# Performance work log

Hardware: AMD Instinct MI355X
Metric: run time of the kernel (lower is better)

Reference implementation:

```python
import jax, jax.numpy as jnp
import numpy as np

B, S, H, A, E, ED, RH = 16, 2048, 1024, 32, 8, 256, 128  # batch, seq, hidden, act_dim, num_experts, expert_dim, router/aux hidden

def _mk(key, shape, scale=0.02):
    return (jax.random.normal(key, shape, dtype=jnp.float32) * scale)

def setup_inputs() -> dict:
    key = jax.random.key(0)
    ks = jax.random.split(key, 20)
    inp = {
        "state_rep": jax.random.normal(ks[0], (B, S, H), dtype=jnp.float32),
        "base_action": jax.random.normal(ks[1], (B, S, A), dtype=jnp.float32),
        "attention_mask": jnp.ones((B, S), dtype=jnp.float32),
        # shared expert
        "sw1": _mk(ks[2], (H, ED)), "sb1": jnp.zeros((ED,), jnp.float32),
        "sw2": _mk(ks[3], (ED, A)), "sb2": jnp.zeros((A,), jnp.float32),
        # stacked specialized experts
        "ew1": _mk(ks[4], (E, H, ED)), "eb1": jnp.zeros((E, ED), jnp.float32),
        "ew2": _mk(ks[5], (E, ED, A)), "eb2": jnp.zeros((E, A), jnp.float32),
        # router
        "rw1": _mk(ks[6], (H, RH)), "rb1": jnp.zeros((RH,), jnp.float32),
        "rw2": _mk(ks[7], (RH, E)), "rb2": jnp.zeros((E,), jnp.float32),
        # residual mlp
        "mw1": _mk(ks[8], (A, RH)), "mb1": jnp.zeros((RH,), jnp.float32),
        "mw2": _mk(ks[9], (RH, A)), "mb2": jnp.zeros((A,), jnp.float32),
        # value estimator
        "vw1": _mk(ks[10], (H, RH)), "vb1": jnp.zeros((RH,), jnp.float32),
        "vw2": _mk(ks[11], (RH, 1)), "vb2": jnp.zeros((1,), jnp.float32),
    }
    return inp

def reference(state_rep, base_action, attention_mask,
              sw1, sb1, sw2, sb2, ew1, eb1, ew2, eb2,
              rw1, rb1, rw2, rb2, mw1, mb1, mw2, mb2,
              vw1, vb1, vw2, vb2):
    gelu = lambda x: jax.nn.gelu(x, approximate=False)  # torch nn.GELU default (erf)
    # value estimator -> sigmoid RTG  [B,S,1]
    return_rtg = jax.nn.sigmoid(jax.nn.relu(state_rep @ vw1 + vb1) @ vw2 + vb2)
    # shared expert [B,S,A]
    shared_output = gelu(state_rep @ sw1 + sb1) @ sw2 + sb2
    # candidate actions [B,S,E,A]
    scaling = jnp.linspace(0.8, 1.2, E, dtype=jnp.float32).reshape(1, 1, E, 1)
    candidate_actions = base_action[:, :, None, :] * scaling
    # router softmax [B,S,E]
    router_logits = gelu(state_rep @ rw1 + rb1) @ rw2 + rb2
    selection_probs = jax.nn.softmax(router_logits, axis=-1)
    # all experts on all tokens (matches the training-mode torch loop)
    h1 = gelu(jnp.einsum('bsh,ehd->bsed', state_rep, ew1) + eb1[None, None, :, :])
    expert_outputs = jnp.einsum('bsed,eda->bsea', h1, ew2) + eb2[None, None, :, :]
    # training branch: soft combine
    weighted_expert = jnp.sum(selection_probs[..., None] * expert_outputs, axis=2)
    moe_output = shared_output + weighted_expert
    residual = gelu(moe_output @ mw1 + mb1) @ mw2 + mb2
    final_action = weighted_expert + residual
    final_action = final_action * attention_mask[..., None]
    return (final_action, candidate_actions, selection_probs, return_rtg)
```

## Files before the change

kernel.cpp:

```cpp
#include <hip/hip_runtime.h>
#include <stdint.h>

#define T_TOT 32768
#define H_DIM 1024
#define A_DIM 32
#define E_NUM 8
#define ED_DIM 256
#define RH_DIM 128
#define NBIG 2560
#define K2 2304

typedef float f32x4 __attribute__((ext_vector_type(4)));
typedef short bf16x8 __attribute__((ext_vector_type(8)));
typedef unsigned short u16;
typedef u16 u16x8 __attribute__((ext_vector_type(8)));

typedef uint32_t __attribute__((address_space(1))) as1_u32;
typedef uint32_t __attribute__((address_space(3))) as3_u32;

__device__ __forceinline__ u16 f2bf(float f) {
    union { float f; uint32_t u; } v; v.f = f;
    return (u16)((v.u + 0x7FFFu + ((v.u >> 16) & 1u)) >> 16);
}
__device__ __forceinline__ float bf2f(u16 h) {
    union { uint32_t u; float f; } v; v.u = ((uint32_t)h) << 16;
    return v.f;
}
__device__ __forceinline__ float gelu_fast(float x) {
    const float x2 = x * x;
    const float s = x * fmaf(0.07135481627f, x2, 1.5957691216f);
    const float e = __expf(-s);
    return x * __builtin_amdgcn_rcpf(1.0f + e);
}
__device__ __forceinline__ void gload_lds16(const void* g, void* lds) {
    __builtin_amdgcn_global_load_lds((const as1_u32*)(uintptr_t)g,
                                     (as3_u32*)(uintptr_t)lds, 16, 0, 0);
}


__global__ void k_packwt(const float* __restrict__ ew1, const float* __restrict__ sw1,
                         const float* __restrict__ rw1, const float* __restrict__ vw1,
                         u16* __restrict__ wbf) {
    __shared__ float t[64][65];
    const int nt = blockIdx.x >> 4, kt = blockIdx.x & 15;
    const int n0 = nt * 64, k0 = kt * 64;
    const int tx = threadIdx.x & 63, ty = threadIdx.x >> 6;
#pragma unroll 4
    for (int it = 0; it < 16; ++it) {
        const int k = k0 + ty + it * 4;
        const int n = n0 + tx;
        float v;
        if (n0 < 2048)      v = ew1[(size_t)((n0 >> 8) * H_DIM + k) * ED_DIM + (n & 255)];
        else if (n0 < 2304) v = sw1[(size_t)k * ED_DIM + (n - 2048)];
        else if (n0 < 2432) v = rw1[(size_t)k * RH_DIM + (n - 2304)];
        else                v = vw1[(size_t)k * RH_DIM + (n - 2432)];
        t[ty + it * 4][tx] = v;
    }
    __syncthreads();
#pragma unroll 4
    for (int it = 0; it < 16; ++it) {
        const int nl = ty + it * 4;
        wbf[(size_t)(n0 + nl) * H_DIM + k0 + tx] = f2bf(t[tx][nl]);
    }
}


#define SB_W2T (A_DIM * K2)
#define SB_W1B (SB_W2T + 4096)
#define SB_W2B (SB_W1B + 4352)
#define SB_BIA (SB_W2B + NBIG)
#define SB_CND (SB_BIA + T_TOT * E_NUM * A_DIM)

__global__ void k_setup(const float* __restrict__ eb1, const float* __restrict__ sb1,
                        const float* __restrict__ rb1, const float* __restrict__ vb1,
                        const float* __restrict__ ew2, const float* __restrict__ sw2,
                        const float* __restrict__ mw1, const float* __restrict__ mw2,
                        const float* __restrict__ base, const float* __restrict__ state,
                        float* __restrict__ biascat,
                        u16* __restrict__ w2t, u16* __restrict__ w1b, u16* __restrict__ w2b,
                        float* __restrict__ cand_out, u16* __restrict__ xb, int nconv4) {
    int i = blockIdx.x * blockDim.x + threadIdx.x;
    if (i < SB_W2T) {
        int a = i / K2, d = i - a * K2;
        float v = (d < 2048) ? ew2[(size_t)d * A_DIM + a] : sw2[(size_t)(d - 2048) * A_DIM + a];
        w2t[i] = f2bf(v);
    } else if (i < SB_W1B) {
        int t = i - SB_W2T;
        w1b[t] = f2bf(mw1[t]);
    } else if (i < SB_W2B) {
        int t = i - SB_W1B;
        int c = t / 136, j = t - c * 136;
        w2b[t] = (j < RH_DIM) ? f2bf(mw2[(size_t)j * A_DIM + c]) : (u16)0;
    } else if (i < SB_BIA) {
        int n = i - SB_W2B;
        float b;
        if (n < 2048)      b = eb1[(n >> 8) * ED_DIM + (n & 255)];
        else if (n < 2304) b = sb1[n - 2048];
        else if (n < 2432) b = rb1[n - 2304];
        else               b = vb1[n - 2432];
        biascat[n] = b;
    } else if (i < SB_CND) {
        int t = i - SB_BIA;
        int a = t & 31, e = (t >> 5) & 7, tt = t >> 8;
        cand_out[t] = base[(size_t)tt * A_DIM + a] * (0.8f + 0.4f * (float)e / 7.0f);
    } else if (i < SB_CND + nconv4) {
        int t = i - SB_CND;
        float4 v = ((const float4*)state)[t];
        ushort4 o;
        o.x = f2bf(v.x); o.y = f2bf(v.y); o.z = f2bf(v.z); o.w = f2bf(v.w);
        ((ushort4*)xb)[t] = o;
    }
}

__global__ void k_convert_x(const float* __restrict__ x, u16* __restrict__ xb, int n4) {
    int i = blockIdx.x * blockDim.x + threadIdx.x;
    if (i >= n4) return;
    float4 v = ((const float4*)x)[i];
    ushort4 o;
    o.x = f2bf(v.x); o.y = f2bf(v.y); o.z = f2bf(v.z); o.w = f2bf(v.w);
    ((ushort4*)xb)[i] = o;
}


#define SLOT 8192

__launch_bounds__(512, 2)
__global__ void k_gemm1(const u16* __restrict__ xb, const u16* __restrict__ wbf,
                        const float* __restrict__ biascat, const u16* __restrict__ w2t,
                        float* __restrict__ Pb,
                        const float* __restrict__ rw2, const float* __restrict__ rb2,
                        const float* __restrict__ vw2, const float* __restrict__ vb2,
                        float* __restrict__ probs_out, float* __restrict__ rtg_out) {
    __shared__ u16 smem[8 * SLOT];
    __shared__ float rw2s[RH_DIM * E_NUM];
    __shared__ float vws[RH_DIM];
    __shared__ float rb2s[E_NUM];
    const int tid = threadIdx.x;
    const int wid = tid >> 6;
    const int lane = tid & 63;
    const int lin = blockIdx.x;
    const int swz = (lin & 7) * ((int)gridDim.x >> 3) + (lin >> 3);
    const int bx = swz % 10;
    const int by = swz / 10;
    const int m0 = by * 256, n0 = bx * 256;
    const int wr = wid >> 2;
    const int wc = wid & 3;
    const int srow = tid >> 3;
    const int cs = 8 * ((tid & 7) ^ (srow & 7));
    const int l15 = lane & 15;
    const int rsw = (lane & 7) * 8;
    const int lh8 = (lane >> 4) * 8;
    const int c0 = lh8 ^ rsw;
    const int c1 = (32 + lh8) ^ rsw;
    const int aRd = (wr * 16 + l15) * 64;
    const int bRd = ((wc & 1) * 64 + l15) * 64;
    const int bSlotHi = wc >> 1;

    f32x4 acc[8][4];
#pragma unroll
    for (int j = 0; j < 8; ++j)
#pragma unroll
        for (int n = 0; n < 4; ++n) acc[j][n] = (f32x4){0.f, 0.f, 0.f, 0.f};

    auto stageA = [&](int h, int kt, int s) {
        const u16* src = xb + (size_t)(m0 + h * 128 + srow) * H_DIM + kt * 64 + cs;
        u16* dst = smem + s * SLOT + wid * 512;
        gload_lds16(src, dst);
        gload_lds16(src + (size_t)64 * H_DIM, dst + 4096);
    };
    auto stageB = [&](int h, int kt, int s) {
        const u16* src = wbf + (size_t)(n0 + h * 128 + srow) * H_DIM + kt * 64 + cs;
        u16* dst = smem + s * SLOT + wid * 512;
        gload_lds16(src, dst);
        gload_lds16(src + (size_t)64 * H_DIM, dst + 4096);
    };

    bf16x8 bfr[4][2];

#define G1_READA(q, P, A0, A1)                                                    \
    {                                                                             \
        const u16* ab0 = smem + ((P) * 4 + ((q) >> 1)) * SLOT + aRd + (((2*(q)) & 3) * 2048);     \
        const u16* ab1 = smem + ((P) * 4 + ((q) >> 1)) * SLOT + aRd + (((2*(q)+1) & 3) * 2048);   \
        A0[0] = *(const bf16x8*)&ab0[c0]; A0[1] = *(const bf16x8*)&ab0[c1];       \
        A1[0] = *(const bf16x8*)&ab1[c0]; A1[1] = *(const bf16x8*)&ab1[c1];       \
    }

#define G1_MFMA(q, A0, A1)                                                        \
    _Pragma("unroll")                                                             \
    for (int ni = 0; ni < 4; ++ni) {                                              \
        acc[2*(q)][ni]   = __builtin_amdgcn_mfma_f32_16x16x32_bf16(A0[0], bfr[ni][0], acc[2*(q)][ni], 0, 0, 0);   \
        acc[2*(q)][ni]   = __builtin_amdgcn_mfma_f32_16x16x32_bf16(A0[1], bfr[ni][1], acc[2*(q)][ni], 0, 0, 0);   \
        acc[2*(q)+1][ni] = __builtin_amdgcn_mfma_f32_16x16x32_bf16(A1[0], bfr[ni][0], acc[2*(q)+1][ni], 0, 0, 0); \
        acc[2*(q)+1][ni] = __builtin_amdgcn_mfma_f32_16x16x32_bf16(A1[1], bfr[ni][1], acc[2*(q)+1][ni], 0, 0, 0); \
    }

    stageB(0, 0, 2); stageB(1, 0, 3);
    stageA(0, 0, 0); stageA(1, 0, 1);
    stageB(0, 1, 6); stageB(1, 1, 7);
    asm volatile("s_waitcnt vmcnt(6)" ::: "memory");
    __builtin_amdgcn_s_barrier();

#pragma unroll 2
    for (int kt = 0; kt < 16; ++kt) {
        const int p = kt & 1;
        const int ktA = (kt + 1) & 15;
        const int ktB = (kt + 2) & 15;
        const int pA = ktA & 1;
        bf16x8 a0[2], a1[2];
        G1_READA(0, p, a0, a1)
#pragma unroll
        for (int ni = 0; ni < 4; ++ni) {
            const u16* bb = smem + (p * 4 + 2 + bSlotHi) * SLOT + bRd + ni * 1024;
            bfr[ni][0] = *(const bf16x8*)&bb[c0];
            bfr[ni][1] = *(const bf16x8*)&bb[c1];
        }
        stageA(0, ktA, pA * 4);
        __builtin_amdgcn_s_barrier();
        asm volatile("s_waitcnt lgkmcnt(0)" ::: "memory");
        __builtin_amdgcn_sched_barrier(0);
        __builtin_amdgcn_s_setprio(1);
        G1_MFMA(0, a0, a1)
        __builtin_amdgcn_s_setprio(0);
        G1_READA(1, p, a0, a1)
        stageA(1, ktA, pA * 4 + 1);
        asm volatile("s_waitcnt vmcnt(8)" ::: "memory");
        __builtin_amdgcn_s_barrier();
        asm volatile("s_waitcnt lgkmcnt(0)" ::: "memory");
        __builtin_amdgcn_sched_barrier(0);
        __builtin_amdgcn_s_setprio(1);
        G1_MFMA(1, a0, a1)
        __builtin_amdgcn_s_setprio(0);
        G1_READA(2, p, a0, a1)
        stageB(0, ktB, p * 4 + 2);
        __builtin_amdgcn_s_barrier();
        asm volatile("s_waitcnt lgkmcnt(0)" ::: "memory");
        __builtin_amdgcn_sched_barrier(0);
        __builtin_amdgcn_s_setprio(1);
        G1_MFMA(2, a0, a1)
        __builtin_amdgcn_s_setprio(0);
        G1_READA(3, p, a0, a1)
        stageB(1, ktB, p * 4 + 3);
        asm volatile("s_waitcnt vmcnt(6)" ::: "memory");
        __builtin_amdgcn_s_barrier();
        asm volatile("s_waitcnt lgkmcnt(0)" ::: "memory");
        __builtin_amdgcn_sched_barrier(0);
        __builtin_amdgcn_s_setprio(1);
        G1_MFMA(3, a0, a1)
        __builtin_amdgcn_s_setprio(0);
    }
#undef G1_READA
#undef G1_MFMA

    const int crow = (lane >> 4) * 4;
    __syncthreads();
    if (bx != 9) {
#pragma unroll
        for (int j = 0; j < 8; ++j) {
#pragma unroll
            for (int ni = 0; ni < 4; ++ni) {
                const int col = wc * 64 + ni * 16 + l15;
                const float bias = biascat[n0 + col];
#pragma unroll
                for (int r = 0; r < 4; ++r) {
                    const int row = wr * 16 + j * 32 + crow + r;
                    const float v = gelu_fast(acc[j][ni][r] + bias);
                    smem[row * 256 + ((((col >> 3) ^ (row & 15)) << 3) | (col & 7))] = f2bf(v);
                }
            }
        }
        __syncthreads();
        f32x4 accP[2][2];
#pragma unroll
        for (int m = 0; m < 2; ++m)
#pragma unroll
            for (int n = 0; n < 2; ++n) accP[m][n] = (f32x4){0.f, 0.f, 0.f, 0.f};
        const int lh16 = lane >> 4;
#pragma unroll
        for (int g = 0; g < 8; ++g) {
            bf16x8 bv[2], av[2];
#pragma unroll
            for (int ni = 0; ni < 2; ++ni)
                bv[ni] = *(const bf16x8*)(w2t + (size_t)(ni * 16 + l15) * K2 + n0 + g * 32 + lh16 * 8);
#pragma unroll
            for (int m = 0; m < 2; ++m) {
                const int row = wid * 32 + m * 16 + l15;
                av[m] = *(const bf16x8*)&smem[row * 256 + (((g * 4 + lh16) ^ l15) << 3)];
            }
#pragma unroll
            for (int m = 0; m < 2; ++m)
#pragma unroll
                for (int ni = 0; ni < 2; ++ni)
                    accP[m][ni] = __builtin_amdgcn_mfma_f32_16x16x32_bf16(av[m], bv[ni], accP[m][ni], 0, 0, 0);
        }
#pragma unroll
        for (int m = 0; m < 2; ++m)
#pragma unroll
            for (int ni = 0; ni < 2; ++ni)
#pragma unroll
                for (int r = 0; r < 4; ++r) {
                    const int row = m0 + wid * 32 + m * 16 + crow + r;
                    Pb[((size_t)row * 9 + bx) * 32 + ni * 16 + l15] = accP[m][ni][r];
                }
    } else {
        for (int i = tid; i < RH_DIM * E_NUM; i += 512) rw2s[i] = rw2[i];
        if (tid < RH_DIM) vws[tid] = vw2[tid];
        if (tid < E_NUM) rb2s[tid] = rb2[tid];
        char* sb = (char*)smem;
#pragma unroll
        for (int j = 0; j < 8; ++j) {
#pragma unroll
            for (int ni = 0; ni < 4; ++ni) {
                const int col = wc * 64 + ni * 16 + l15;
                const float bias = biascat[2304 + col];
#pragma unroll
                for (int r = 0; r < 4; ++r) {
                    const int row = wr * 16 + j * 32 + crow + r;
                    float v = acc[j][ni][r] + bias;
                    v = (col < 128) ? gelu_fast(v) : fmaxf(v, 0.f);
                    *(u16*)(sb + row * 512 + ((col * 2) ^ ((row & 31) << 4))) = f2bf(v);
                }
            }
        }
        __syncthreads();
        if (tid < 256) {
            const int row = tid;
            float lg[E_NUM];
#pragma unroll
            for (int e = 0; e < E_NUM; ++e) lg[e] = rb2s[e];
            const int rx = (row & 31) << 4;
#pragma unroll 4
            for (int s = 0; s < 16; ++s) {
                u16x8 v8 = *(const u16x8*)(sb + row * 512 + ((s << 4) ^ rx));
#pragma unroll
                for (int q = 0; q < 8; ++q) {
                    const float xv = bf2f(v8[q]);
                    const float* wr8 = &rw2s[(s * 8 + q) * E_NUM];
#pragma unroll
                    for (int e = 0; e < E_NUM; ++e) lg[e] = fmaf(xv, wr8[e], lg[e]);
                }
            }
            float mx = lg[0];
#pragma unroll
            for (int e = 1; e < E_NUM; ++e) mx = fmaxf(mx, lg[e]);
            float sm = 0.f;
            float ex[E_NUM];
#pragma unroll
            for (int e = 0; e < E_NUM; ++e) { ex[e] = __expf(lg[e] - mx); sm += ex[e]; }
            const float rs = 1.0f / sm;
#pragma unroll
            for (int e = 0; e < E_NUM; ++e) probs_out[(size_t)(m0 + row) * E_NUM + e] = ex[e] * rs;
        } else {
            const int row = tid - 256;
            const int rx = (row & 31) << 4;
            float pv = 0.f;
#pragma unroll 4
            for (int s = 16; s < 32; ++s) {
                u16x8 v8 = *(const u16x8*)(sb + row * 512 + ((s << 4) ^ rx));
#pragma unroll
                for (int q = 0; q < 8; ++q) pv = fmaf(bf2f(v8[q]), vws[(s - 16) * 8 + q], pv);
            }
            rtg_out[m0 + row] = 1.f / (1.f + __expf(-(pv + vb2[0])));
        }
    }
}


__launch_bounds__(256, 3)
__global__ void k_combine(const float* __restrict__ Pb, const float* __restrict__ probs,
                          const float* __restrict__ eb2, const float* __restrict__ sb2,
                          const u16* __restrict__ w1b, const u16* __restrict__ w2b,
                          const float* __restrict__ mb1, const float* __restrict__ mb2,
                          const float* __restrict__ mask, float* __restrict__ out_final) {
    __shared__ float plds[64 * E_NUM];
    __shared__ u16 Am[64 * 40];
    __shared__ u16 rhm[64 * 136];
    __shared__ u16 w1s[32 * 128];
    __shared__ u16 w2s[32 * 136];
    const int tid = threadIdx.x;
    const int wid = tid >> 6;
    const int lane = tid & 63;
    const int m0 = blockIdx.x * 64;
    const int crow = (lane >> 4) * 4;
    const int ccol = lane & 15;

    for (int i = tid; i < 64 * E_NUM; i += 256) plds[i] = probs[(size_t)m0 * E_NUM + i];
    for (int i = tid; i < 4096; i += 256) w1s[i] = w1b[i];
    for (int i = tid; i < 544; i += 256) *(u16x8*)&w2s[i * 8] = *(const u16x8*)&w2b[i * 8];
    __syncthreads();

    float wgt[2][4];
#pragma unroll
    for (int n = 0; n < 2; ++n) {
        const int aIdx = n * 16 + ccol;
#pragma unroll
        for (int r = 0; r < 4; ++r) {
            const int row = wid * 16 + crow + r;
            const float* pt = Pb + (size_t)(m0 + row) * 288;
            float w = 0.f;
#pragma unroll
            for (int e = 0; e < E_NUM; ++e)
                w = fmaf(plds[row * E_NUM + e], pt[e * 32 + aIdx] + eb2[e * A_DIM + aIdx], w);
            wgt[n][r] = w;
            Am[row * 40 + aIdx] = f2bf(w + pt[256 + aIdx] + sb2[aIdx]);
        }
    }
    __syncthreads();
    {
        const int row = tid >> 2, seg = tid & 3;
        float mrow[32];
#pragma unroll
        for (int a = 0; a < 32; ++a) mrow[a] = bf2f(Am[row * 40 + a]);
#pragma unroll 4
        for (int jj = 0; jj < 32; ++jj) {
            const int j = seg * 32 + jj;
            float s = mb1[j];
#pragma unroll
            for (int a = 0; a < 32; ++a) s = fmaf(mrow[a], bf2f(w1s[a * 128 + j]), s);
            rhm[row * 136 + j] = f2bf(gelu_fast(s));
        }
    }
    __syncthreads();
#pragma unroll
    for (int n = 0; n < 2; ++n) {
        const int aIdx = n * 16 + ccol;
        const float b2 = mb2[aIdx];
#pragma unroll
        for (int r = 0; r < 4; ++r) {
            const int row = wid * 16 + crow + r;
            float s = b2;
#pragma unroll
            for (int jc = 0; jc < 16; ++jc) {
                u16x8 rv = *(const u16x8*)&rhm[row * 136 + jc * 8];
                u16x8 wv = *(const u16x8*)&w2s[aIdx * 136 + jc * 8];
#pragma unroll
                for (int q = 0; q < 8; ++q) s = fmaf(bf2f(rv[q]), bf2f(wv[q]), s);
            }
            const int t = m0 + row;
            out_final[(size_t)t * A_DIM + aIdx] = (wgt[n][r] + s) * mask[t];
        }
    }
}


extern "C" void kernel_launch(void* const* d_in, const int* in_sizes, int n_in,
                              void* d_out, int out_size, void* d_ws, size_t ws_size,
                              hipStream_t stream) {
    const float* state = (const float*)d_in[0];
    const float* base  = (const float*)d_in[1];
    const float* mask  = (const float*)d_in[2];
    const float* sw1 = (const float*)d_in[3];
    const float* sb1 = (const float*)d_in[4];
    const float* sw2 = (const float*)d_in[5];
    const float* sb2 = (const float*)d_in[6];
    const float* ew1 = (const float*)d_in[7];
    const float* eb1 = (const float*)d_in[8];
    const float* ew2 = (const float*)d_in[9];
    const float* eb2 = (const float*)d_in[10];
    const float* rw1 = (const float*)d_in[11];
    const float* rb1 = (const float*)d_in[12];
    const float* rw2 = (const float*)d_in[13];
    const float* rb2 = (const float*)d_in[14];
    const float* mw1 = (const float*)d_in[15];
    const float* mb1 = (const float*)d_in[16];
    const float* mw2 = (const float*)d_in[17];
    const float* mb2 = (const float*)d_in[18];
    const float* vw1 = (const float*)d_in[19];
    const float* vb1 = (const float*)d_in[20];
    const float* vw2 = (const float*)d_in[21];
    const float* vb2 = (const float*)d_in[22];

    float* out_final = (float*)d_out;
    float* out_cand  = out_final + 1048576;
    float* out_probs = out_final + 9437184;
    float* out_rtg   = out_final + 9699328;

    auto al = [](size_t b) { return (b + 255) & ~(size_t)255; };
    auto need = [&](size_t T) {
        return al((size_t)NBIG * H_DIM * 2) + al((size_t)A_DIM * K2 * 2) + al((size_t)NBIG * 4)
             + al((size_t)4096 * 2) + al((size_t)4352 * 2)
             + al(T * H_DIM * 2) + al(T * 9 * A_DIM * 4);
    };
    size_t Tc = 8192;
    if (need(32768) <= ws_size)      Tc = 32768;
    else if (need(16384) <= ws_size) Tc = 16384;
    const int nchunk = (int)(T_TOT / Tc);

    char* ws = (char*)d_ws;
    size_t off = 0;
    auto take = [&](size_t b) { char* p = ws + off; off += (b + 255) & ~(size_t)255; return p; };
    u16*   wbf   = (u16*)take((size_t)NBIG * H_DIM * 2);
    u16*   w2t   = (u16*)take((size_t)A_DIM * K2 * 2);
    float* bias  = (float*)take((size_t)NBIG * 4);
    u16*   w1b   = (u16*)take((size_t)4096 * 2);
    u16*   w2b   = (u16*)take((size_t)4352 * 2);
    u16*   xb    = (u16*)take(Tc * H_DIM * 2);
    float* Pb    = (float*)take(Tc * 9 * A_DIM * 4);
    (void)in_sizes; (void)n_in; (void)out_size;

    const int nconv4 = (Tc == 32768) ? (T_TOT * H_DIM / 4) : 0;
    const int ntot = SB_CND + nconv4;
    k_packwt<<<640, 256, 0, stream>>>(ew1, sw1, rw1, vw1, wbf);
    k_setup<<<(ntot + 255) / 256, 256, 0, stream>>>(
        eb1, sb1, rb1, vb1, ew2, sw2, mw1, mw2,
        base, state, bias, w2t, w1b, w2b, out_cand, xb, nconv4);

    for (int c = 0; c < nchunk; ++c) {
        const size_t tb = (size_t)c * Tc;
        if (nconv4 == 0)
            k_convert_x<<<(int)(Tc * H_DIM / 4 / 256), 256, 0, stream>>>(state + tb * H_DIM, xb, (int)(Tc * H_DIM / 4));
        k_gemm1<<<10 * (int)(Tc / 256), 512, 0, stream>>>(xb, wbf, bias, w2t, Pb,
                                                          rw2, rb2, vw2, vb2,
                                                          out_probs + tb * E_NUM, out_rtg + tb);
        k_combine<<<(int)(Tc / 64), 256, 0, stream>>>(Pb, out_probs + tb * E_NUM, eb2, sb2,
                                                      w1b, w2b, mb1, mb2, mask + tb, out_final + tb * A_DIM);
    }
}
```

Measured before the change: 274.8 us.

## Merge weight packing into setup, vectorize conversions, store expert partials as bf16

Folds the weight transpose/pack kernel into the setup kernel as extra blocks, which removes one launch and lets both run concurrently. The candidate-action and state-to-bf16 conversion loops now handle 4 and 8 elements per thread. The intermediate per-expert partial outputs buffer is stored as bf16 instead of fp32, halving its write and read traffic between the GEMM and combine kernels. The trade-off is extra rounding on the expert outputs before the weighted combine.

After: 251.3 us. 8.6% less time.

```diff
diff --git a/kernel.cpp b/kernel.cpp
--- a/kernel.cpp
+++ b/kernel.cpp
@@ -38,77 +38,84 @@
 }
 
 
-__global__ void k_packwt(const float* __restrict__ ew1, const float* __restrict__ sw1,
-                         const float* __restrict__ rw1, const float* __restrict__ vw1,
-                         u16* __restrict__ wbf) {
-    __shared__ float t[64][65];
-    const int nt = blockIdx.x >> 4, kt = blockIdx.x & 15;
-    const int n0 = nt * 64, k0 = kt * 64;
-    const int tx = threadIdx.x & 63, ty = threadIdx.x >> 6;
-#pragma unroll 4
-    for (int it = 0; it < 16; ++it) {
-        const int k = k0 + ty + it * 4;
-        const int n = n0 + tx;
-        float v;
-        if (n0 < 2048)      v = ew1[(size_t)((n0 >> 8) * H_DIM + k) * ED_DIM + (n & 255)];
-        else if (n0 < 2304) v = sw1[(size_t)k * ED_DIM + (n - 2048)];
-        else if (n0 < 2432) v = rw1[(size_t)k * RH_DIM + (n - 2304)];
-        else                v = vw1[(size_t)k * RH_DIM + (n - 2432)];
-        t[ty + it * 4][tx] = v;
-    }
-    __syncthreads();
-#pragma unroll 4
-    for (int it = 0; it < 16; ++it) {
-        const int nl = ty + it * 4;
-        wbf[(size_t)(n0 + nl) * H_DIM + k0 + tx] = f2bf(t[tx][nl]);
-    }
-}
-
-
-#define SB_W2T (A_DIM * K2)
-#define SB_W1B (SB_W2T + 4096)
-#define SB_W2B (SB_W1B + 4352)
-#define SB_BIA (SB_W2B + NBIG)
-#define SB_CND (SB_BIA + T_TOT * E_NUM * A_DIM)
-
-__global__ void k_setup(const float* __restrict__ eb1, const float* __restrict__ sb1,
+#define PW_BLKS 640
+#define C0 (A_DIM * K2)
+#define C1 (C0 + 4096)
+#define C2 (C1 + 4352)
+#define C3 (C2 + NBIG)
+#define C4 (C3 + T_TOT * E_NUM * A_DIM / 4)
+
+__global__ void k_setup(const float* __restrict__ ew1, const float* __restrict__ sw1,
+                        const float* __restrict__ rw1, const float* __restrict__ vw1,
+                        const float* __restrict__ eb1, const float* __restrict__ sb1,
                         const float* __restrict__ rb1, const float* __restrict__ vb1,
                         const float* __restrict__ ew2, const float* __restrict__ sw2,
                         const float* __restrict__ mw1, const float* __restrict__ mw2,
                         const float* __restrict__ base, const float* __restrict__ state,
-                        float* __restrict__ biascat,
+                        u16* __restrict__ wbf, float* __restrict__ biascat,
                         u16* __restrict__ w2t, u16* __restrict__ w1b, u16* __restrict__ w2b,
-                        float* __restrict__ cand_out, u16* __restrict__ xb, int nconv4) {
-    int i = blockIdx.x * blockDim.x + threadIdx.x;
-    if (i < SB_W2T) {
+                        float* __restrict__ cand_out, u16* __restrict__ xb, int nconv8) {
+    __shared__ float t[64][65];
+    if (blockIdx.x < PW_BLKS) {
+        const int nt = blockIdx.x >> 4, kt = blockIdx.x & 15;
+        const int n0 = nt * 64, k0 = kt * 64;
+        const int tx = threadIdx.x & 63, ty = threadIdx.x >> 6;
+#pragma unroll 4
+        for (int it = 0; it < 16; ++it) {
+            const int k = k0 + ty + it * 4;
+            const int n = n0 + tx;
+            float v;
+            if (n0 < 2048)      v = ew1[(size_t)((n0 >> 8) * H_DIM + k) * ED_DIM + (n & 255)];
+            else if (n0 < 2304) v = sw1[(size_t)k * ED_DIM + (n - 2048)];
+            else if (n0 < 2432) v = rw1[(size_t)k * RH_DIM + (n - 2304)];
+            else                v = vw1[(size_t)k * RH_DIM + (n - 2432)];
+            t[ty + it * 4][tx] = v;
+        }
+        __syncthreads();
+#pragma unroll 4
+        for (int it = 0; it < 16; ++it) {
+            const int nl = ty + it * 4;
+            wbf[(size_t)(n0 + nl) * H_DIM + k0 + tx] = f2bf(t[tx][nl]);
+        }
+        return;
+    }
+    const int i = (blockIdx.x - PW_BLKS) * 256 + threadIdx.x;
+    if (i < C0) {
         int a = i / K2, d = i - a * K2;
         float v = (d < 2048) ? ew2[(size_t)d * A_DIM + a] : sw2[(size_t)(d - 2048) * A_DIM + a];
         w2t[i] = f2bf(v);
-    } else if (i < SB_W1B) {
-        int t = i - SB_W2T;
-        w1b[t] = f2bf(mw1[t]);
-    } else if (i < SB_W2B) {
-        int t = i - SB_W1B;
-        int c = t / 136, j = t - c * 136;
-        w2b[t] = (j < RH_DIM) ? f2bf(mw2[(size_t)j * A_DIM + c]) : (u16)0;
-    } else if (i < SB_BIA) {
-        int n = i - SB_W2B;
+    } else if (i < C1) {
+        int q = i - C0;
+        w1b[q] = f2bf(mw1[q]);
+    } else if (i < C2) {
+        int q = i - C1;
+        int c = q / 136, j = q - c * 136;
+        w2b[q] = (j < RH_DIM) ? f2bf(mw2[(size_t)j * A_DIM + c]) : (u16)0;
+    } else if (i < C3) {
+        int n = i - C2;
         float b;
         if (n < 2048)      b = eb1[(n >> 8) * ED_DIM + (n & 255)];
         else if (n < 2304) b = sb1[n - 2048];
         else if (n < 2432) b = rb1[n - 2304];
         else               b = vb1[n - 2432];
         biascat[n] = b;
-    } else if (i < SB_CND) {
-        int t = i - SB_BIA;
-        int a = t & 31, e = (t >> 5) & 7, tt = t >> 8;
-        cand_out[t] = base[(size_t)tt * A_DIM + a] * (0.8f + 0.4f * (float)e / 7.0f);
-    } else if (i < SB_CND + nconv4) {
-        int t = i - SB_CND;
-        float4 v = ((const float4*)state)[t];
-        ushort4 o;
-        o.x = f2bf(v.x); o.y = f2bf(v.y); o.z = f2bf(v.z); o.w = f2bf(v.w);
-        ((ushort4*)xb)[t] = o;
+    } else if (i < C4) {
+        const int t4 = i - C3;
+        const int g = t4 * 4;
+        const int e = (g >> 5) & 7;
+        const float scl = 0.8f + 0.4f * (float)e / 7.0f;
+        const int bidx = ((g >> 8) * A_DIM + (g & 31)) >> 2;
+        float4 v = ((const float4*)base)[bidx];
+        v.x *= scl; v.y *= scl; v.z *= scl; v.w *= scl;
+        ((float4*)cand_out)[t4] = v;
+    } else if (i < C4 + nconv8) {
+        const int q = i - C4;
+        float4 v0 = ((const float4*)state)[q * 2];
+        float4 v1 = ((const float4*)state)[q * 2 + 1];
+        u16x8 o;
+        o[0] = f2bf(v0.x); o[1] = f2bf(v0.y); o[2] = f2bf(v0.z); o[3] = f2bf(v0.w);
+        o[4] = f2bf(v1.x); o[5] = f2bf(v1.y); o[6] = f2bf(v1.z); o[7] = f2bf(v1.w);
+        ((u16x8*)xb)[q] = o;
     }
 }
 
@@ -127,7 +134,7 @@
 __launch_bounds__(512, 2)
 __global__ void k_gemm1(const u16* __restrict__ xb, const u16* __restrict__ wbf,
                         const float* __restrict__ biascat, const u16* __restrict__ w2t,
-                        float* __restrict__ Pb,
+                        u16* __restrict__ Pb,
                         const float* __restrict__ rw2, const float* __restrict__ rb2,
                         const float* __restrict__ vw2, const float* __restrict__ vb2,
                         float* __restrict__ probs_out, float* __restrict__ rtg_out) {
@@ -299,7 +306,7 @@
 #pragma unroll
                 for (int r = 0; r < 4; ++r) {
                     const int row = m0 + wid * 32 + m * 16 + crow + r;
-                    Pb[((size_t)row * 9 + bx) * 32 + ni * 16 + l15] = accP[m][ni][r];
+                    Pb[((size_t)row * 9 + bx) * 32 + ni * 16 + l15] = f2bf(accP[m][ni][r]);
                 }
     } else {
         for (int i = tid; i < RH_DIM * E_NUM; i += 512) rw2s[i] = rw2[i];
@@ -366,7 +373,7 @@
 
 
 __launch_bounds__(256, 3)
-__global__ void k_combine(const float* __restrict__ Pb, const float* __restrict__ probs,
+__global__ void k_combine(const u16* __restrict__ Pb, const float* __restrict__ probs,
                           const float* __restrict__ eb2, const float* __restrict__ sb2,
                           const u16* __restrict__ w1b, const u16* __restrict__ w2b,
                           const float* __restrict__ mb1, const float* __restrict__ mb2,
@@ -395,13 +402,13 @@
 #pragma unroll
         for (int r = 0; r < 4; ++r) {
             const int row = wid * 16 + crow + r;
-            const float* pt = Pb + (size_t)(m0 + row) * 288;
+            const u16* pt = Pb + (size_t)(m0 + row) * 288;
             float w = 0.f;
 #pragma unroll
             for (int e = 0; e < E_NUM; ++e)
-                w = fmaf(plds[row * E_NUM + e], pt[e * 32 + aIdx] + eb2[e * A_DIM + aIdx], w);
+                w = fmaf(plds[row * E_NUM + e], bf2f(pt[e * 32 + aIdx]) + eb2[e * A_DIM + aIdx], w);
             wgt[n][r] = w;
-            Am[row * 40 + aIdx] = f2bf(w + pt[256 + aIdx] + sb2[aIdx]);
+            Am[row * 40 + aIdx] = f2bf(w + bf2f(pt[256 + aIdx]) + sb2[aIdx]);
         }
     }
     __syncthreads();
@@ -478,7 +485,7 @@
     auto need = [&](size_t T) {
         return al((size_t)NBIG * H_DIM * 2) + al((size_t)A_DIM * K2 * 2) + al((size_t)NBIG * 4)
              + al((size_t)4096 * 2) + al((size_t)4352 * 2)
-             + al(T * H_DIM * 2) + al(T * 9 * A_DIM * 4);
+             + al(T * H_DIM * 2) + al(T * 9 * A_DIM * 2);
     };
     size_t Tc = 8192;
     if (need(32768) <= ws_size)      Tc = 32768;
@@ -494,19 +501,18 @@
     u16*   w1b   = (u16*)take((size_t)4096 * 2);
     u16*   w2b   = (u16*)take((size_t)4352 * 2);
     u16*   xb    = (u16*)take(Tc * H_DIM * 2);
-    float* Pb    = (float*)take(Tc * 9 * A_DIM * 4);
+    u16*   Pb    = (u16*)take(Tc * 9 * A_DIM * 2);
     (void)in_sizes; (void)n_in; (void)out_size;
 
-    const int nconv4 = (Tc == 32768) ? (T_TOT * H_DIM / 4) : 0;
-    const int ntot = SB_CND + nconv4;
-    k_packwt<<<640, 256, 0, stream>>>(ew1, sw1, rw1, vw1, wbf);
-    k_setup<<<(ntot + 255) / 256, 256, 0, stream>>>(
-        eb1, sb1, rb1, vb1, ew2, sw2, mw1, mw2,
-        base, state, bias, w2t, w1b, w2b, out_cand, xb, nconv4);
+    const int nconv8 = (Tc == 32768) ? (T_TOT * H_DIM / 8) : 0;
+    const int flat_blocks = (C4 + nconv8 + 255) / 256;
+    k_setup<<<PW_BLKS + flat_blocks, 256, 0, stream>>>(
+        ew1, sw1, rw1, vw1, eb1, sb1, rb1, vb1, ew2, sw2, mw1, mw2,
+        base, state, wbf, bias, w2t, w1b, w2b, out_cand, xb, nconv8);
 
     for (int c = 0; c < nchunk; ++c) {
         const size_t tb = (size_t)c * Tc;
-        if (nconv4 == 0)
+        if (nconv8 == 0)
             k_convert_x<<<(int)(Tc * H_DIM / 4 / 256), 256, 0, stream>>>(state + tb * H_DIM, xb, (int)(Tc * H_DIM / 4));
         k_gemm1<<<10 * (int)(Tc / 256), 512, 0, stream>>>(xb, wbf, bias, w2t, Pb,
                                                           rw2, rb2, vw2, vb2,
```
